# Optimization experiments

Measured on AMD Instinct MI355X. Metric: run time of the kernel, lower is better.

The kernel has to match this reference:

```python
import jax, jax.numpy as jnp
import numpy as np

EMB_DIM = 1024
HEAD_NUM = 16
HEAD_DIM = EMB_DIM // HEAD_NUM
B, S = 2, 2048


def setup_inputs() -> dict:
    key = jax.random.key(0)
    k_x, k_wqkv, k_bqkv, k_wo, k_bo = jax.random.split(key, 5)
    x = jax.random.normal(k_x, (B, S, EMB_DIM), dtype=jnp.float32)
    # nn.Linear default init scale ~ 1/sqrt(fan_in); exact distribution irrelevant for a reference
    lim = 1.0 / np.sqrt(EMB_DIM)
    W_qkv = jax.random.uniform(k_wqkv, (EMB_DIM, 3 * EMB_DIM), jnp.float32, -lim, lim)
    b_qkv = jax.random.uniform(k_bqkv, (3 * EMB_DIM,), jnp.float32, -lim, lim)
    W_o = jax.random.uniform(k_wo, (EMB_DIM, EMB_DIM), jnp.float32, -lim, lim)
    b_o = jax.random.uniform(k_bo, (EMB_DIM,), jnp.float32, -lim, lim)
    mask = jnp.tril(jnp.ones((S, S), dtype=bool))  # causal mask as in casual_mask(seq_len)
    return {"x": x, "W_qkv": W_qkv, "b_qkv": b_qkv, "W_o": W_o, "b_o": b_o, "mask": mask}


def reference(x, W_qkv, b_qkv, W_o, b_o, mask):
    b, s, e = x.shape
    qkv = x @ W_qkv + b_qkv                      # [b, s, 3e]
    q, k, v = qkv[..., :e], qkv[..., e:2 * e], qkv[..., 2 * e:]
    # [b, s, h, d] -> [b, h, s, d]
    q = q.reshape(b, s, HEAD_NUM, HEAD_DIM).transpose(0, 2, 1, 3)
    k = k.reshape(b, s, HEAD_NUM, HEAD_DIM).transpose(0, 2, 1, 3)
    v = v.reshape(b, s, HEAD_NUM, HEAD_DIM).transpose(0, 2, 1, 3)
    scores = jnp.einsum("bhqd,bhkd->bhqk", q, k) / jnp.sqrt(jnp.float32(HEAD_DIM))
    scores = jnp.where(mask, scores, -jnp.inf)   # masked_fill(~mask, -inf)
    probs = jax.nn.softmax(scores, axis=-1)      # dropout is identity in eval mode
    out = jnp.einsum("bhqk,bhkd->bhqd", probs, v)
    out = out.transpose(0, 2, 1, 3).reshape(b, s, e)
    return out @ W_o + b_o
```

## Files before the change

kernel.cpp:

```cpp
#include <hip/hip_runtime.h>


typedef __attribute__((ext_vector_type(8))) short short8;
typedef __attribute__((ext_vector_type(4))) short short4v;
typedef __attribute__((ext_vector_type(4))) float floatx4;

#define NB 2
#define SEQ 2048
#define EMB 1024
#define NH 16
#define HD 64
#define M_ROWS (NB * SEQ)
#define N_QKV (3 * EMB)

#define GLL(g, l) __builtin_amdgcn_global_load_lds( \
    (const __attribute__((address_space(1))) void*)(g), \
    (__attribute__((address_space(3))) void*)(l), 16, 0, 0)

#if defined(__HIP_DEVICE_COMPILE__)
#define MFMA16K16(A, B, C) __builtin_amdgcn_mfma_f32_16x16x16bf16_1k(A, B, C, 0, 0, 0)
#else
#define MFMA16K16(A, B, C) (C)
#endif

static __device__ __forceinline__ unsigned short f2bf(float f) {
    union { float f; unsigned int u; } v; v.f = f;
    unsigned int r = v.u + 0x7FFFu + ((v.u >> 16) & 1u);
    return (unsigned short)(r >> 16);
}
static __device__ __forceinline__ float bf2f(unsigned short h) {
    union { unsigned int u; float f; } v; v.u = ((unsigned int)h) << 16;
    return v.f;
}

static __device__ __forceinline__ unsigned int cvt_pk_bf16(float lo, float hi) {
#if defined(__HIP_DEVICE_COMPILE__)
    unsigned int r;
    asm("v_cvt_pk_bf16_f32 %0, %1, %2" : "=v"(r) : "v"(lo), "v"(hi));
    return r;
#else
    (void)lo; (void)hi; return 0u;
#endif
}
static __device__ __forceinline__ short4v pack4bf(float a, float b, float c, float d) {
    union { unsigned int u[2]; short4v s; } pu;
    pu.u[0] = cvt_pk_bf16(a, b);
    pu.u[1] = cvt_pk_bf16(c, d);
    return pu.s;
}

__global__ void prep(const float* __restrict__ x,
                     const float* __restrict__ Wqkv, const float* __restrict__ Wo,
                     unsigned short* __restrict__ x_bf,
                     unsigned short* __restrict__ wqkvT, unsigned short* __restrict__ woT) {
    __shared__ unsigned short tile[32][33];
    int z = blockIdx.z;
    int tx = threadIdx.x, ty = threadIdx.y;
    if (z == 2) {
        int id = ((int)blockIdx.y * 96 + (int)blockIdx.x) * 256 + ty * 32 + tx;
        const int n4 = M_ROWS * EMB / 4;
        for (int i = id; i < n4; i += 96 * 32 * 256) {
            float4 v = ((const float4*)x)[i];
            unsigned long long p = (unsigned long long)f2bf(v.x)
                | ((unsigned long long)f2bf(v.y) << 16)
                | ((unsigned long long)f2bf(v.z) << 32)
                | ((unsigned long long)f2bf(v.w) << 48);
            ((unsigned long long*)x_bf)[i] = p;
        }
        return;
    }
    int C = z ? EMB : N_QKV;
    if ((int)blockIdx.x * 32 >= C) return;
    const float* in = z ? Wo : Wqkv;
    unsigned short* out = z ? woT : wqkvT;
    const int R = EMB;
    int c0 = blockIdx.x * 32, r0 = blockIdx.y * 32;
    #pragma unroll
    for (int j = 0; j < 4; ++j)
        tile[ty + j * 8][tx] = f2bf(in[(size_t)(r0 + ty + j * 8) * C + c0 + tx]);
    __syncthreads();
    #pragma unroll
    for (int j = 0; j < 4; ++j)
        out[(size_t)(c0 + ty + j * 8) * R + r0 + tx] = tile[tx][ty + j * 8];
}

#define CTS 130

__global__ __launch_bounds__(256) void qkv_gemm(
    const unsigned short* __restrict__ A,
    const unsigned short* __restrict__ Bt,
    const float* __restrict__ bias,
    unsigned short* __restrict__ qb, unsigned short* __restrict__ kb,
    unsigned short* __restrict__ vb)
{
    const int K = EMB;
    __shared__ __align__(16) unsigned short smem[128 * CTS];

    int t = threadIdx.x;
    int m0 = blockIdx.y * 128;
    int n0 = blockIdx.x * 128;
    int w = t >> 6, lane = t & 63, quad = lane >> 4, lcol = lane & 15;
    int wr = w >> 1, wc = w & 1;

    floatx4 zero = {0.f, 0.f, 0.f, 0.f};
    floatx4 acc[4][4];
    #pragma unroll
    for (int i = 0; i < 4; ++i)
        #pragma unroll
        for (int j = 0; j < 4; ++j) acc[i][j] = zero;

    const unsigned short* a0 = A  + (size_t)(m0 + (t >> 2)) * K + ((t & 3) << 3);
    const unsigned short* b0 = Bt + (size_t)(n0 + (t >> 2)) * K + ((t & 3) << 3);
    unsigned short* la = &smem[t << 3];

    GLL(a0, la);
    GLL(a0 + 64 * K, la + 2048);
    GLL(b0, la + 4096);
    GLL(b0 + 64 * K, la + 6144);

    for (int k0 = 0; k0 < K; k0 += 32) {
        int cur = (k0 >> 5) & 1, nxt = cur ^ 1;
        __syncthreads();
        if (k0 + 32 < K) {
            GLL(a0 + k0 + 32, la + nxt * 8192);
            GLL(a0 + 64 * K + k0 + 32, la + nxt * 8192 + 2048);
            GLL(b0 + k0 + 32, la + nxt * 8192 + 4096);
            GLL(b0 + 64 * K + k0 + 32, la + nxt * 8192 + 6144);
        }
        const unsigned short* As = &smem[cur * 8192];
        const unsigned short* Bs = As + 4096;
        short8 af[4], bfm[4];
        #pragma unroll
        for (int i = 0; i < 4; ++i)
            af[i] = *(const short8*)(&As[(wr * 64 + i * 16 + lcol) * 32 + quad * 8]);
        #pragma unroll
        for (int j = 0; j < 4; ++j)
            bfm[j] = *(const short8*)(&Bs[(wc * 64 + j * 16 + lcol) * 32 + quad * 8]);
        #pragma unroll
        for (int i = 0; i < 4; ++i)
            #pragma unroll
            for (int j = 0; j < 4; ++j)
                acc[i][j] = __builtin_amdgcn_mfma_f32_16x16x32_bf16(af[i], bfm[j], acc[i][j], 0, 0, 0);
    }

    bool isV = (n0 >= 2 * EMB);
    __syncthreads();
    #pragma unroll
    for (int i = 0; i < 4; ++i) {
        int row0 = wr * 64 + i * 16 + quad * 4;
        #pragma unroll
        for (int j = 0; j < 4; ++j) {
            int col = wc * 64 + j * 16 + lcol;
            float bv = bias[n0 + col];
            #pragma unroll
            for (int r = 0; r < 4; ++r) {
                unsigned short hv = f2bf(acc[i][j][r] + bv);
                if (isV) smem[col * CTS + row0 + r] = hv;
                else     smem[(row0 + r) * CTS + col] = hv;
            }
        }
    }
    __syncthreads();

    int b = m0 >> 11, s0 = m0 & 2047;
    int hbase = (n0 & 1023) >> 6;
    if (!isV) {
        unsigned short* dst = (n0 >= EMB) ? kb : qb;
        #pragma unroll
        for (int it = 0; it < 8; ++it) {
            int job = it * 32 + (t >> 3);
            int tok = job & 127, hh = job >> 7;
            int chunk = t & 7;
            short8 vv = *(const short8*)(&smem[tok * CTS + hh * 64 + chunk * 8]);
            size_t g = ((size_t)((b * NH + hbase + hh) * SEQ + s0 + tok)) * HD + chunk * 8;
            *(short8*)(&dst[g]) = vv;
        }
    } else {
        #pragma unroll
        for (int it = 0; it < 8; ++it) {
            int job = it * 32 + (t >> 3);
            int f = job & 127, half = job >> 7;
            int chunk = (t & 7) + half * 8;
            short8 vv = *(const short8*)(&smem[f * CTS + chunk * 8]);
            int h = hbase + (f >> 6), d = f & 63;
            size_t g = ((size_t)((b * NH + h) * HD + d)) * SEQ + s0 + chunk * 8;
            *(short8*)(&vb[g]) = vv;
        }
    }
}

__global__ __launch_bounds__(256) void attn_fused(
    const unsigned short* __restrict__ Q,
    const unsigned short* __restrict__ Kk,
    const unsigned short* __restrict__ Vt,
    unsigned short* __restrict__ Out)
{
    __shared__ __align__(16) unsigned short Ks[2][64 * 64];
    __shared__ __align__(16) unsigned short Vs[2][64 * 64];

    int n = (int)blockIdx.y * 16 + (int)blockIdx.x;
    int hi = n >> 8;
    int j = n & 255;
    int idx = j >> 3;
    int bh = (j & 7) * 4 + (idx & 3);
    int qpre = idx >> 2;
    int qt2 = hi ? (15 - qpre) : qpre;

    int q0 = qt2 * 128;
    int ktEnd = 2 * (qt2 + 1);

    int t = threadIdx.x;
    int w = t >> 6, lane = t & 63, quad = lane >> 4, lcol = lane & 15;
    const size_t hoff = (size_t)bh * SEQ * HD;
    const float SC = 0.18033688011112043f;

    short8 aq[2][2];
    #pragma unroll
    for (int g = 0; g < 2; ++g) {
        const unsigned short* qp = Q + hoff
            + (size_t)(q0 + g * 64 + 16 * w + lcol) * HD + quad * 8;
        aq[g][0] = *(const short8*)qp;
        aq[g][1] = *(const short8*)(qp + 32);
    }

    int srow = t >> 3;
    int ss   = (t & 7) ^ (srow & 7);
    const unsigned short* kgl = Kk + hoff + (size_t)srow * HD + ss * 8;
    const unsigned short* vgl = Vt + hoff + (size_t)srow * SEQ + ss * 8;
    unsigned short* kld = &Ks[0][t * 8];
    unsigned short* vld = &Vs[0][t * 8];

    floatx4 zero = {0.f, 0.f, 0.f, 0.f};
    floatx4 O[2][4];
    floatx4 lacc[2];
    #pragma unroll
    for (int g = 0; g < 2; ++g) {
        lacc[g] = zero;
        #pragma unroll
        for (int td = 0; td < 4; ++td) O[g][td] = zero;
    }

    short4v ones4;
    #pragma unroll
    for (int jj = 0; jj < 4; ++jj) ones4[jj] = (short)0x3F80;

    {
        GLL(kgl, kld);
        GLL(kgl + (size_t)32 * HD, kld + 2048);
        GLL(vgl, vld);
        GLL(vgl + (size_t)32 * SEQ, vld + 2048);
    }

    int sx0 = (quad ^ (lcol & 7)) << 3;
    int sx1 = sx0 ^ 32;

    for (int kt = 0; kt < ktEnd; ++kt) {
        int cur = kt & 1, nxt = cur ^ 1;
        __syncthreads();
        if (kt + 1 < ktEnd) {
            int k0 = (kt + 1) * 64;
            GLL(kgl + (size_t)k0 * HD, kld + nxt * 4096);
            GLL(kgl + (size_t)(k0 + 32) * HD, kld + nxt * 4096 + 2048);
            GLL(vgl + k0, vld + nxt * 4096);
            GLL(vgl + (size_t)32 * SEQ + k0, vld + nxt * 4096 + 2048);
        }

        const unsigned short* ksr = &Ks[cur][0];
        const unsigned short* vsr = &Vs[cur][0];
        short8 bk0[4], bk1[4];
        #pragma unroll
        for (int tc = 0; tc < 4; ++tc) {
            int rb = (tc * 16 + lcol) << 6;
            bk0[tc] = *(const short8*)(ksr + rb + sx0);
            bk1[tc] = *(const short8*)(ksr + rb + sx1);
        }

        short4v pk[2][4];
        bool act[2];
        #pragma unroll
        for (int g = 0; g < 2; ++g) {
            const int gb = q0 + g * 64 + 16 * w;
            act[g] = (kt * 64 <= gb + 15);
            if (act[g]) {
                floatx4 sacc[4];
                #pragma unroll
                for (int tc = 0; tc < 4; ++tc) {
                    sacc[tc] = __builtin_amdgcn_mfma_f32_16x16x32_bf16(bk0[tc], aq[g][0], zero, 0, 0, 0);
                    sacc[tc] = __builtin_amdgcn_mfma_f32_16x16x32_bf16(bk1[tc], aq[g][1], sacc[tc], 0, 0, 0);
                }
                if (kt * 64 + 63 > gb) {
                    int qrow = gb + lcol;
                    #pragma unroll
                    for (int tc = 0; tc < 4; ++tc) {
                        float p[4];
                        #pragma unroll
                        for (int r = 0; r < 4; ++r) {
                            float e = __builtin_amdgcn_exp2f(sacc[tc][r] * SC);
                            p[r] = (kt * 64 + tc * 16 + quad * 4 + r > qrow) ? 0.f : e;
                        }
                        pk[g][tc] = pack4bf(p[0], p[1], p[2], p[3]);
                    }
                } else {
                    #pragma unroll
                    for (int tc = 0; tc < 4; ++tc) {
                        pk[g][tc] = pack4bf(
                            __builtin_amdgcn_exp2f(sacc[tc][0] * SC),
                            __builtin_amdgcn_exp2f(sacc[tc][1] * SC),
                            __builtin_amdgcn_exp2f(sacc[tc][2] * SC),
                            __builtin_amdgcn_exp2f(sacc[tc][3] * SC));
                    }
                }
            }
        }

        #pragma unroll
        for (int td = 0; td < 4; ++td) {
            short4v va[4];
            #pragma unroll
            for (int tc = 0; tc < 4; ++tc) {
                int seg = ((tc << 1) + (quad >> 1)) ^ (lcol & 7);
                va[tc] = *(const short4v*)(vsr + ((td * 16 + lcol) << 6) + (seg << 3) + ((quad & 1) << 2));
            }
            if (act[0]) {
                #pragma unroll
                for (int tc = 0; tc < 4; ++tc)
                    O[0][td] = MFMA16K16(va[tc], pk[0][tc], O[0][td]);
            }
            if (act[1]) {
                #pragma unroll
                for (int tc = 0; tc < 4; ++tc)
                    O[1][td] = MFMA16K16(va[tc], pk[1][tc], O[1][td]);
            }
        }
        #pragma unroll
        for (int g = 0; g < 2; ++g) {
            if (act[g]) {
                #pragma unroll
                for (int tc = 0; tc < 4; ++tc)
                    lacc[g] = MFMA16K16(ones4, pk[g][tc], lacc[g]);
            }
        }
    }

    int b = bh >> 4, h = bh & 15;
    #pragma unroll
    for (int g = 0; g < 2; ++g) {
        int qrow = q0 + g * 64 + 16 * w + lcol;
        float inv = 1.0f / lacc[g][0];
        size_t obase = ((size_t)b * SEQ + qrow) * EMB + (size_t)h * HD + quad * 4;
        #pragma unroll
        for (int td = 0; td < 4; ++td) {
            short4v ov;
            #pragma unroll
            for (int r = 0; r < 4; ++r) ov[r] = (short)f2bf(O[g][td][r] * inv);
            *(short4v*)(&Out[obase + td * 16]) = ov;
        }
    }
}

__global__ __launch_bounds__(256) void oproj_gemm(
    const unsigned short* __restrict__ A,
    const unsigned short* __restrict__ Bt,
    const float* __restrict__ bias,
    float* __restrict__ Cout)
{
    const int K = EMB;
    __shared__ __align__(16) unsigned short smem[2 * 8192];
    int t = threadIdx.x;
    int m0 = blockIdx.y * 128;
    int n0 = blockIdx.x * 128;
    int w = t >> 6, lane = t & 63, quad = lane >> 4, lcol = lane & 15;
    int wr = w >> 1, wc = w & 1;

    floatx4 zero = {0.f, 0.f, 0.f, 0.f};
    floatx4 acc[4][4];
    #pragma unroll
    for (int i = 0; i < 4; ++i)
        #pragma unroll
        for (int j = 0; j < 4; ++j) acc[i][j] = zero;

    const unsigned short* a0 = A  + (size_t)(m0 + (t >> 2)) * K + ((t & 3) << 3);
    const unsigned short* b0 = Bt + (size_t)(n0 + (t >> 2)) * K + ((t & 3) << 3);
    unsigned short* la = &smem[t << 3];

    GLL(a0, la);
    GLL(a0 + 64 * K, la + 2048);
    GLL(b0, la + 4096);
    GLL(b0 + 64 * K, la + 6144);

    for (int k0 = 0; k0 < K; k0 += 32) {
        int cur = (k0 >> 5) & 1, nxt = cur ^ 1;
        __syncthreads();
        if (k0 + 32 < K) {
            GLL(a0 + k0 + 32, la + nxt * 8192);
            GLL(a0 + 64 * K + k0 + 32, la + nxt * 8192 + 2048);
            GLL(b0 + k0 + 32, la + nxt * 8192 + 4096);
            GLL(b0 + 64 * K + k0 + 32, la + nxt * 8192 + 6144);
        }
        const unsigned short* As = &smem[cur * 8192];
        const unsigned short* Bs = As + 4096;
        short8 af[4], bfm[4];
        #pragma unroll
        for (int i = 0; i < 4; ++i)
            af[i] = *(const short8*)(&As[(wr * 64 + i * 16 + lcol) * 32 + quad * 8]);
        #pragma unroll
        for (int j = 0; j < 4; ++j)
            bfm[j] = *(const short8*)(&Bs[(wc * 64 + j * 16 + lcol) * 32 + quad * 8]);
        #pragma unroll
        for (int i = 0; i < 4; ++i)
            #pragma unroll
            for (int j = 0; j < 4; ++j)
                acc[i][j] = __builtin_amdgcn_mfma_f32_16x16x32_bf16(af[i], bfm[j], acc[i][j], 0, 0, 0);
    }

    #pragma unroll
    for (int i = 0; i < 4; ++i) {
        int m = m0 + wr * 64 + i * 16 + quad * 4;
        #pragma unroll
        for (int j = 0; j < 4; ++j) {
            int n = n0 + wc * 64 + j * 16 + lcol;
            float bv = bias[n];
            #pragma unroll
            for (int r = 0; r < 4; ++r)
                Cout[(size_t)(m + r) * EMB + n] = acc[i][j][r] + bv;
        }
    }
}

extern "C" void kernel_launch(void* const* d_in, const int* in_sizes, int n_in,
                              void* d_out, int out_size, void* d_ws, size_t ws_size,
                              hipStream_t stream) {
    (void)in_sizes; (void)n_in; (void)out_size; (void)ws_size;
    char* ws = (char*)d_ws;
    const size_t OFF_X     = 0;
    const size_t OFF_WQKVT = OFF_X     + (size_t)M_ROWS * EMB * 2;
    const size_t OFF_WOT   = OFF_WQKVT + (size_t)N_QKV * EMB * 2;
    const size_t OFF_Q     = OFF_WOT   + (size_t)EMB * EMB * 2;
    const size_t OFF_K     = OFF_Q     + (size_t)M_ROWS * EMB * 2;
    const size_t OFF_V     = OFF_K     + (size_t)M_ROWS * EMB * 2;
    const size_t OFF_ATTN  = OFF_V     + (size_t)M_ROWS * EMB * 2;

    const float* x    = (const float*)d_in[0];
    const float* Wqkv = (const float*)d_in[1];
    const float* bqkv = (const float*)d_in[2];
    const float* Wo   = (const float*)d_in[3];
    const float* bo   = (const float*)d_in[4];

    unsigned short* x_bf  = (unsigned short*)(ws + OFF_X);
    unsigned short* wqkvT = (unsigned short*)(ws + OFF_WQKVT);
    unsigned short* woT   = (unsigned short*)(ws + OFF_WOT);
    unsigned short* qb    = (unsigned short*)(ws + OFF_Q);
    unsigned short* kb    = (unsigned short*)(ws + OFF_K);
    unsigned short* vb    = (unsigned short*)(ws + OFF_V);
    unsigned short* attn  = (unsigned short*)(ws + OFF_ATTN);

    prep<<<dim3(96, 32, 3), dim3(32, 8), 0, stream>>>(x, Wqkv, Wo, x_bf, wqkvT, woT);

    qkv_gemm<<<dim3(N_QKV / 128, M_ROWS / 128), 256, 0, stream>>>(x_bf, wqkvT, bqkv, qb, kb, vb);
    attn_fused<<<dim3(16, NB * NH), 256, 0, stream>>>(qb, kb, vb, attn);
    oproj_gemm<<<dim3(EMB / 128, M_ROWS / 128), 256, 0, stream>>>(attn, woT, bo, (float*)d_out);
}
```

Before: 197.8 us.

## Split long causal attention query tiles across multiple blocks with a combine pass

Attention query tiles with many key tiles are split into 1-4 chunks along the key dimension, which turns 512 blocks into 1280 roughly balanced ones ordered by a constant lookup table. Partial unnormalized outputs and row sums go to workspace slots (reusing the x_bf region), and a new combine kernel sums them and normalizes. The change targets causal load imbalance and the long tail of the attention kernel. In exchange it adds partial-result traffic, an extra launch, and bf16 rounding of the partial sums. It also sets an occupancy hint of 5 blocks per CU in launch bounds.

```diff
diff --git a/kernel.cpp b/kernel.cpp
--- a/kernel.cpp
+++ b/kernel.cpp
@@ -12,6 +12,8 @@
 #define HD 64
 #define M_ROWS (NB * SEQ)
 #define N_QKV (3 * EMB)
+#define SLOT_B 16896
+#define SLOTS_PER_BH 24
 
 #define GLL(g, l) __builtin_amdgcn_global_load_lds( \
     (const __attribute__((address_space(1))) void*)(g), \
@@ -47,6 +49,21 @@
     pu.u[0] = cvt_pk_bf16(a, b);
     pu.u[1] = cvt_pk_bf16(c, d);
     return pu.s;
+}
+
+__constant__ unsigned char FQT[40] = {
+    3,11,14,15,15, 9,12,13,  7,11,14,15, 6, 9,12,13,
+    7,11,15, 5, 6,10,13,14, 10, 2, 4, 5, 8,10,13,14,
+    0, 1, 4, 8, 8, 9,12,12 };
+__constant__ unsigned char FCI[40] = {
+    0, 0, 1, 1, 3, 1, 1, 2,  0, 1, 3, 2, 0, 2, 3, 3,
+    1, 2, 0, 0, 1, 0, 0, 0,  2, 0, 0, 1, 1, 1, 1, 2,
+    0, 0, 1, 0, 2, 0, 0, 2 };
+
+static __device__ __forceinline__ int slot_off(int qt2, int ci) {
+    int so = (qt2 < 8) ? (qt2 - 4)
+           : (qt2 < 12 ? 4 + (qt2 - 8) * 2 : 12 + (qt2 - 12) * 3);
+    return so + (ci - 1);
 }
 
 __global__ void prep(const float* __restrict__ x,
@@ -189,25 +206,26 @@
     }
 }
 
-__global__ __launch_bounds__(256) void attn_fused(
+__global__ __launch_bounds__(256, 5) void attn_fused(
     const unsigned short* __restrict__ Q,
     const unsigned short* __restrict__ Kk,
     const unsigned short* __restrict__ Vt,
-    unsigned short* __restrict__ Out)
+    unsigned short* __restrict__ Out,
+    unsigned char* __restrict__ Part,
+    float* __restrict__ Laux)
 {
     __shared__ __align__(16) unsigned short Ks[2][64 * 64];
     __shared__ __align__(16) unsigned short Vs[2][64 * 64];
 
-    int n = (int)blockIdx.y * 16 + (int)blockIdx.x;
-    int hi = n >> 8;
-    int j = n & 255;
-    int idx = j >> 3;
-    int bh = (j & 7) * 4 + (idx & 3);
-    int qpre = idx >> 2;
-    int qt2 = hi ? (15 - qpre) : qpre;
-
-    int q0 = qt2 * 128;
-    int ktEnd = 2 * (qt2 + 1);
+    int fid = (int)blockIdx.y * 40 + (int)blockIdx.x;
+    int bh  = (fid & 7) * 4 + ((fid >> 3) & 3);
+    int qq  = fid >> 5;
+    int qt2 = FQT[qq];
+    int ci  = FCI[qq];
+    int nc  = 1 + (qt2 >> 2);
+    int nt  = 2 * (qt2 + 1);
+    int t0  = (nt * ci) / nc, t1 = (nt * (ci + 1)) / nc;
+    int q0  = qt2 * 128;
 
     int t = threadIdx.x;
     int w = t >> 6, lane = t & 63, quad = lane >> 4, lcol = lane & 15;
@@ -245,22 +263,24 @@
     for (int jj = 0; jj < 4; ++jj) ones4[jj] = (short)0x3F80;
 
     {
-        GLL(kgl, kld);
-        GLL(kgl + (size_t)32 * HD, kld + 2048);
-        GLL(vgl, vld);
-        GLL(vgl + (size_t)32 * SEQ, vld + 2048);
+        int pb = (t0 & 1) * 4096;
+        size_t k0 = (size_t)t0 * 64;
+        GLL(kgl + k0 * HD, kld + pb);
+        GLL(kgl + (k0 + 32) * HD, kld + pb + 2048);
+        GLL(vgl + k0, vld + pb);
+        GLL(vgl + (size_t)32 * SEQ + k0, vld + pb + 2048);
     }
 
     int sx0 = (quad ^ (lcol & 7)) << 3;
     int sx1 = sx0 ^ 32;
 
-    for (int kt = 0; kt < ktEnd; ++kt) {
+    for (int kt = t0; kt < t1; ++kt) {
         int cur = kt & 1, nxt = cur ^ 1;
         __syncthreads();
-        if (kt + 1 < ktEnd) {
-            int k0 = (kt + 1) * 64;
-            GLL(kgl + (size_t)k0 * HD, kld + nxt * 4096);
-            GLL(kgl + (size_t)(k0 + 32) * HD, kld + nxt * 4096 + 2048);
+        if (kt + 1 < t1) {
+            size_t k0 = (size_t)(kt + 1) * 64;
+            GLL(kgl + k0 * HD, kld + nxt * 4096);
+            GLL(kgl + (k0 + 32) * HD, kld + nxt * 4096 + 2048);
             GLL(vgl + k0, vld + nxt * 4096);
             GLL(vgl + (size_t)32 * SEQ + k0, vld + nxt * 4096 + 2048);
         }
@@ -342,19 +362,95 @@
         }
     }
 
+    if (nc == 1) {
+        int b = bh >> 4, h = bh & 15;
+        #pragma unroll
+        for (int g = 0; g < 2; ++g) {
+            int qrow = q0 + g * 64 + 16 * w + lcol;
+            float inv = 1.0f / lacc[g][0];
+            size_t obase = ((size_t)b * SEQ + qrow) * EMB + (size_t)h * HD + quad * 4;
+            #pragma unroll
+            for (int td = 0; td < 4; ++td) {
+                short4v ov;
+                #pragma unroll
+                for (int r = 0; r < 4; ++r) ov[r] = (short)f2bf(O[g][td][r] * inv);
+                *(short4v*)(&Out[obase + td * 16]) = ov;
+            }
+        }
+    } else if (ci == 0) {
+        int b = bh >> 4, h = bh & 15;
+        float* lrow = Laux + ((size_t)bh * 12 + (qt2 - 4)) * 128;
+        #pragma unroll
+        for (int g = 0; g < 2; ++g) {
+            int ql = g * 64 + 16 * w + lcol;
+            int qrow = q0 + ql;
+            size_t obase = ((size_t)b * SEQ + qrow) * EMB + (size_t)h * HD + quad * 4;
+            #pragma unroll
+            for (int td = 0; td < 4; ++td) {
+                short4v ov;
+                #pragma unroll
+                for (int r = 0; r < 4; ++r) ov[r] = (short)f2bf(O[g][td][r]);
+                *(short4v*)(&Out[obase + td * 16]) = ov;
+            }
+            if (quad == 0) lrow[ql] = lacc[g][0];
+        }
+    } else {
+        unsigned char* sp = Part
+            + (size_t)(bh * SLOTS_PER_BH + slot_off(qt2, ci)) * SLOT_B;
+        unsigned short* sO = (unsigned short*)sp;
+        float* sL = (float*)(sp + 16384);
+        #pragma unroll
+        for (int g = 0; g < 2; ++g) {
+            int ql = g * 64 + 16 * w + lcol;
+            #pragma unroll
+            for (int td = 0; td < 4; ++td) {
+                short4v ov;
+                #pragma unroll
+                for (int r = 0; r < 4; ++r) ov[r] = (short)f2bf(O[g][td][r]);
+                *(short4v*)(&sO[ql * 64 + td * 16 + quad * 4]) = ov;
+            }
+            if (quad == 0) sL[ql] = lacc[g][0];
+        }
+    }
+}
+
+__global__ __launch_bounds__(256) void attn_combine(
+    const unsigned char* __restrict__ Part, const float* __restrict__ Laux,
+    unsigned short* __restrict__ Out)
+{
+    int qt2 = 4 + (int)blockIdx.x;
+    int bh = blockIdx.y;
+    int nc = 1 + (qt2 >> 2);
+    const unsigned char* base = Part
+        + (size_t)(bh * SLOTS_PER_BH + slot_off(qt2, 1)) * SLOT_B;
+    const float* lrow = Laux + ((size_t)bh * 12 + (qt2 - 4)) * 128;
     int b = bh >> 4, h = bh & 15;
-    #pragma unroll
-    for (int g = 0; g < 2; ++g) {
-        int qrow = q0 + g * 64 + 16 * w + lcol;
-        float inv = 1.0f / lacc[g][0];
-        size_t obase = ((size_t)b * SEQ + qrow) * EMB + (size_t)h * HD + quad * 4;
-        #pragma unroll
-        for (int td = 0; td < 4; ++td) {
-            short4v ov;
-            #pragma unroll
-            for (int r = 0; r < 4; ++r) ov[r] = (short)f2bf(O[g][td][r] * inv);
-            *(short4v*)(&Out[obase + td * 16]) = ov;
-        }
+    size_t obase = ((size_t)b * SEQ + qt2 * 128) * EMB + (size_t)h * HD;
+    int t = threadIdx.x;
+    #pragma unroll
+    for (int it = 0; it < 4; ++it) {
+        int job = it * 256 + t;
+        int row = job >> 3, c8 = (job & 7) * 8;
+        unsigned short* op = &Out[obase + (size_t)row * EMB + c8];
+        float acc8[8];
+        short8 v0 = *(const short8*)op;
+        #pragma unroll
+        for (int e = 0; e < 8; ++e) acc8[e] = bf2f((unsigned short)v0[e]);
+        float lsum = lrow[row];
+        for (int k = 1; k < nc; ++k) {
+            const unsigned char* sp = base + (size_t)(k - 1) * SLOT_B;
+            const unsigned short* sO = (const unsigned short*)sp;
+            const float* sL = (const float*)(sp + 16384);
+            short8 vv = *(const short8*)(&sO[row * 64 + c8]);
+            #pragma unroll
+            for (int e = 0; e < 8; ++e) acc8[e] += bf2f((unsigned short)vv[e]);
+            lsum += sL[row];
+        }
+        float inv = 1.0f / lsum;
+        short8 ov;
+        #pragma unroll
+        for (int e = 0; e < 8; ++e) ov[e] = (short)f2bf(acc8[e] * inv);
+        *(short8*)op = ov;
     }
 }
 
@@ -439,6 +535,8 @@
     const size_t OFF_K     = OFF_Q     + (size_t)M_ROWS * EMB * 2;
     const size_t OFF_V     = OFF_K     + (size_t)M_ROWS * EMB * 2;
     const size_t OFF_ATTN  = OFF_V     + (size_t)M_ROWS * EMB * 2;
+    const size_t OFF_PART  = OFF_X;
+    const size_t OFF_LAUX  = OFF_PART + (size_t)32 * SLOTS_PER_BH * SLOT_B;
 
     const float* x    = (const float*)d_in[0];
     const float* Wqkv = (const float*)d_in[1];
@@ -453,10 +551,13 @@
     unsigned short* kb    = (unsigned short*)(ws + OFF_K);
     unsigned short* vb    = (unsigned short*)(ws + OFF_V);
     unsigned short* attn  = (unsigned short*)(ws + OFF_ATTN);
+    unsigned char*  part  = (unsigned char*)(ws + OFF_PART);
+    float*          laux  = (float*)(ws + OFF_LAUX);
 
     prep<<<dim3(96, 32, 3), dim3(32, 8), 0, stream>>>(x, Wqkv, Wo, x_bf, wqkvT, woT);
 
     qkv_gemm<<<dim3(N_QKV / 128, M_ROWS / 128), 256, 0, stream>>>(x_bf, wqkvT, bqkv, qb, kb, vb);
-    attn_fused<<<dim3(16, NB * NH), 256, 0, stream>>>(qb, kb, vb, attn);
+    attn_fused<<<dim3(40, NB * NH), 256, 0, stream>>>(qb, kb, vb, attn, part, laux);
+    attn_combine<<<dim3(12, NB * NH), 256, 0, stream>>>(part, laux, attn);
     oproj_gemm<<<dim3(EMB / 128, M_ROWS / 128), 256, 0, stream>>>(attn, woT, bo, (float*)d_out);
 }
```

Result: slower. 362.3 us (+83.2%).
